# Performance work log

Hardware: AMD Instinct MI355X
Metric: run time of the kernel (lower is better)

## Reference

```python
import jax, jax.numpy as jnp
import numpy as np

THRESH = 0.3
VRESET = 0.0
TAU_M = 3.0
MAX_D = 5
LENS = 0.5  # surrogate-gradient window half-width

B, WIN, N_IN = 512, 100, 700
H1, H2, H3 = 512, 256, 128

@jax.custom_vjp
def spike_fn(mem):
    # Heaviside spike with rectangular surrogate gradient (standard ActFun in SNN repos)
    return (mem > THRESH).astype(mem.dtype)

def _spike_fwd(mem):
    return spike_fn(mem), mem

def _spike_bwd(mem, g):
    return (g * (jnp.abs(mem - THRESH) < LENS).astype(g.dtype),)

spike_fn.defvjp(_spike_fwd, _spike_bwd)


def mem_update(i_spike, o_spike, mem, W, alpha):
    # mem = mem*alpha*(1-o_spike) + W @ i_spike - o_spike*vreset
    mem = mem * alpha * (1.0 - o_spike) + i_spike @ W.T - o_spike * VRESET
    s = spike_fn(mem)
    mem = mem * (mem < THRESH).astype(mem.dtype)  # hard reset above threshold
    return mem, s


def setup_inputs() -> dict:
    key = jax.random.key(0)
    ks = jax.random.split(key, 7)
    x = (jax.random.uniform(ks[0], (B, WIN, N_IN), jnp.float32) > 0.9).astype(jnp.float32)

    def lin(k, fan_out, fan_in):
        bound = 1.0 / np.sqrt(fan_in)
        return jax.random.uniform(k, (fan_out, fan_in), jnp.float32, -bound, bound)

    return {
        "x": x,
        "W_ih1": lin(ks[1], H1, N_IN),
        "W_h1h2": lin(ks[2], H2, H1),
        "W_h2h3": lin(ks[3], H3, H2),
        "W_h3h2": lin(ks[4], H2, H3),
        "W_h2h1": lin(ks[5], H1, H2),
        "W_h1o": lin(ks[6], N_IN, H1),
    }


def reference(x, W_ih1, W_h1h2, W_h2h3, W_h3h2, W_h2h1, W_h1o):
    b, t, n = x.shape
    alpha = jnp.exp(jnp.asarray(-1.0 / TAU_M, x.dtype))
    ext = jnp.concatenate([jnp.zeros((b, MAX_D, n), x.dtype), x], axis=1)  # [B, T+max_d, N]
    xs = jnp.swapaxes(ext, 0, 1)  # [T+max_d, B, N]

    z = lambda d: jnp.zeros((b, d), x.dtype)
    carry0 = (z(H1), z(H1), z(H2), z(H2), z(H3), z(H3),
              z(H2), z(H2), z(H1), z(H1), z(n), z(n))

    def step(carry, xt):
        m1, s1, m2, s2, m3, s3, m2d, s2d, m1d, s1d, mo, so = carry
        m1, s1 = mem_update(xt, s1, m1, W_ih1, alpha)
        m2, s2 = mem_update(s1, s2, m2, W_h1h2, alpha)
        m3, s3 = mem_update(s2, s3, m3, W_h2h3, alpha)
        m2d, s2d = mem_update(s3, s2d, m2d, W_h3h2, alpha)
        m1d, s1d = mem_update(s2d, s1d, m1d, W_h2h1, alpha)
        mo, so = mem_update(s1d, so, mo, W_h1o, alpha)
        return (m1, s1, m2, s2, m3, s3, m2d, s2d, m1d, s1d, mo, so), so

    _, all_o = jax.lax.scan(step, carry0, xs)  # [T+max_d, B, N]
    return jnp.swapaxes(all_o[MAX_D:], 0, 1)   # [B, T, N]
```

## Files before the change

kernel.cpp:

```cpp
#include <hip/hip_runtime.h>
#include <cmath>

namespace {

constexpr int kWin = 100;
constexpr int kNin = 700;

constexpr size_t OFF1 = 0;
constexpr size_t OFF2 = 358400;
constexpr size_t OFF3 = 489472;
constexpr size_t OFF4 = 522240;
constexpr size_t OFF5 = 555008;
constexpr size_t OFF6 = 686080;
constexpr size_t OFF_END = 1044480;
constexpr size_t XM_OFF_U64 = OFF_END / 2;

__global__ void transpose_k(const float* __restrict__ src, float* __restrict__ dst,
                            int H, int K) {
  int idx = blockIdx.x * blockDim.x + threadIdx.x;
  if (idx < H * K) {
    int h = idx / K;
    int k = idx - h * K;
    dst[(size_t)k * H + h] = src[idx];
  }
}

__global__ __launch_bounds__(256) void xmask_k(const float* __restrict__ x,
                                               unsigned long long* __restrict__ xm) {
  const int bid = blockIdx.x;
  const int tid = threadIdx.x;
  const int lane = tid & 63;
  const int wv = tid >> 6;
  const float* xr = x + (size_t)bid * kNin;
  unsigned long long* dst = xm + (size_t)bid * 12;
#pragma unroll
  for (int s = 0; s < 3; ++s) {
    const int h = s * 256 + tid;
    const bool p = (h < kNin) ? (xr[h] != 0.0f) : false;
    const unsigned long long b = __ballot(p);
    if (lane == 0) dst[s * 4 + wv] = b;
  }
}

template <int K, int H, bool BUILD, typename FCh>
__device__ __forceinline__ void lif(const float* __restrict__ WT, FCh&& chunk,
                                    double* mem, unsigned long long* mOut,
                                    double (*part)[3][256],
                                    float* outRow,
                                    int kp, int ht, int lane, int wv4,
                                    double alpha) {
  constexpr int NS = (H + 255) / 256;
  constexpr int NC = (K + 31) / 32;
  double acc[NS];
#pragma unroll
  for (int s = 0; s < NS; ++s) acc[s] = 0.0;

  unsigned mNext = chunk(kp);
  for (int c = kp; c < NC; c += 4) {
    unsigned m = __builtin_amdgcn_readfirstlane(mNext);
    if (c + 4 < NC) mNext = chunk(c + 4);
    const float* __restrict__ cbase = WT + (size_t)c * 32 * H;
    const int cnt = __builtin_popcount(m);
    int i = 0;
    for (; i + 4 <= cnt; i += 4) {
      const int b0 = __builtin_ctz(m); m &= m - 1;
      const int b1 = __builtin_ctz(m); m &= m - 1;
      const int b2 = __builtin_ctz(m); m &= m - 1;
      const int b3 = __builtin_ctz(m); m &= m - 1;
      const float* p0 = cbase + b0 * H;
      const float* p1 = cbase + b1 * H;
      const float* p2 = cbase + b2 * H;
      const float* p3 = cbase + b3 * H;
#pragma unroll
      for (int s = 0; s < NS; ++s) {
        const int h = s * 256 + ht;
        if ((s + 1) * 256 <= H || h < H) {
          const float f0 = p0[h];
          const float f1 = p1[h];
          const float f2 = p2[h];
          const float f3 = p3[h];
          const double t01 = (double)f0 + (double)f1;
          const double t23 = (double)f2 + (double)f3;
          acc[s] += t01 + t23;
        }
      }
    }
    for (; i < cnt; ++i) {
      const int b0 = __builtin_ctz(m); m &= m - 1;
      const float* p0 = cbase + b0 * H;
#pragma unroll
      for (int s = 0; s < NS; ++s) {
        const int h = s * 256 + ht;
        if ((s + 1) * 256 <= H || h < H) acc[s] += (double)p0[h];
      }
    }
  }

#pragma unroll
  for (int s = 0; s < NS; ++s) part[kp][s][ht] = acc[s];
  __syncthreads();

  bool pred[NS];
#pragma unroll
  for (int s = 0; s < NS; ++s) {
    const int h = s * 256 + ht;
    if ((s + 1) * 256 <= H || h < H) {
      const double p01 = part[0][s][ht] + part[1][s][ht];
      const double tot = (p01 + part[2][s][ht]) + part[3][s][ht];
      const double mm = mem[s] * alpha + tot;
      pred[s] = (mm > 0.3);
      mem[s] = (mm < 0.3) ? mm : 0.0;
      if (!BUILD) {
        if (kp == s) outRow[h] = pred[s] ? 1.0f : 0.0f;
      }
    } else {
      pred[s] = false;
    }
  }
  if (BUILD) {
#pragma unroll
    for (int s = 0; s < NS; ++s) {
      const unsigned long long b = __ballot(pred[s]);
      if (kp == 0 && lane == 0) mOut[s * 4 + wv4] = b;
    }
    __syncthreads();
  }
}

__global__ __launch_bounds__(1024, 8) void snn_main(
    const float* __restrict__ wsf, const unsigned long long* __restrict__ xmask,
    float* __restrict__ out) {
  const int tid = threadIdx.x;
  const int kp = tid >> 8;
  const int ht = tid & 255;
  const int lane = tid & 63;
  const int wv4 = (tid >> 6) & 3;
  const int row = blockIdx.x;

  const float* WT1 = wsf + OFF1;
  const float* WT2 = wsf + OFF2;
  const float* WT3 = wsf + OFF3;
  const float* WT4 = wsf + OFF4;
  const float* WT5 = wsf + OFF5;
  const float* WT6 = wsf + OFF6;

  __shared__ unsigned long long mk[2][12];
  __shared__ double parts[2][4][3][256];

  double m1[2] = {0.0, 0.0};
  double m2[1] = {0.0};
  double m3[1] = {0.0};
  double m4[1] = {0.0};
  double m5[2] = {0.0, 0.0};
  double m6[3] = {0.0, 0.0, 0.0};

  const double alpha = exp(-1.0 / 3.0);

  const unsigned long long* xmRow = xmask + (size_t)row * kWin * 12;
  float* outRowBase = out + (size_t)row * kWin * kNin;

  for (int t = 0; t < kWin; ++t) {
    const unsigned* xm32 = (const unsigned*)(xmRow + (size_t)t * 12);
    const unsigned* mk0 = (const unsigned*)&mk[0][0];
    const unsigned* mk1 = (const unsigned*)&mk[1][0];

    lif<700, 512, true>(WT1, [&](int c) { return xm32[c]; }, m1, mk[0],
                        parts[0], nullptr, kp, ht, lane, wv4, alpha);
    lif<512, 256, true>(WT2, [&](int c) { return mk0[c]; }, m2, mk[1],
                        parts[1], nullptr, kp, ht, lane, wv4, alpha);
    lif<256, 128, true>(WT3, [&](int c) { return mk1[c]; }, m3, mk[0],
                        parts[0], nullptr, kp, ht, lane, wv4, alpha);
    lif<128, 256, true>(WT4, [&](int c) { return mk0[c]; }, m4, mk[1],
                        parts[1], nullptr, kp, ht, lane, wv4, alpha);
    lif<256, 512, true>(WT5, [&](int c) { return mk1[c]; }, m5, mk[0],
                        parts[0], nullptr, kp, ht, lane, wv4, alpha);
    float* outRow = outRowBase + (size_t)t * kNin;
    lif<512, 700, false>(WT6, [&](int c) { return mk0[c]; }, m6, nullptr,
                         parts[1], outRow, kp, ht, lane, wv4, alpha);
  }
}

}

extern "C" void kernel_launch(void* const* d_in, const int* in_sizes, int n_in,
                              void* d_out, int out_size, void* d_ws, size_t ws_size,
                              hipStream_t stream) {
  const float* x = (const float*)d_in[0];
  float* ws = (float*)d_ws;
  unsigned long long* xm = (unsigned long long*)d_ws + XM_OFF_U64;
  float* out = (float*)d_out;

  struct TK { int H, K; size_t off; int idx; };
  const TK tk[6] = {
      {512, 700, OFF1, 1},
      {256, 512, OFF2, 2},
      {128, 256, OFF3, 3},
      {256, 128, OFF4, 4},
      {512, 256, OFF5, 5},
      {700, 512, OFF6, 6},
  };
  for (int i = 0; i < 6; ++i) {
    const int n = tk[i].H * tk[i].K;
    transpose_k<<<(n + 255) / 256, 256, 0, stream>>>(
        (const float*)d_in[tk[i].idx], ws + tk[i].off, tk[i].H, tk[i].K);
  }

  xmask_k<<<512 * kWin, 256, 0, stream>>>(x, xm);

  snn_main<<<512, 1024, 0, stream>>>(ws, xm, out);
}
```

Measured before the change: 1.141 ms.

## Balance sparse spike work across K-partitions by splitting active rows evenly

Each of the four K-partition thread groups now takes an equal share of the active spike indices, replacing the earlier round-robin assignment of 32-bit chunks, which could leave groups with very different amounts of work. Spike counts are computed with popcounts when the masks are built, and the last word of the input mask is reused to hold the total count. In exchange, every group now scans all mask chunks from the start, and the bit-skipping loops add scalar work per layer per timestep.

```diff
diff --git a/kernel.cpp b/kernel.cpp
--- a/kernel.cpp
+++ b/kernel.cpp
@@ -33,18 +33,28 @@
   const int wv = tid >> 6;
   const float* xr = x + (size_t)bid * kNin;
   unsigned long long* dst = xm + (size_t)bid * 12;
+  __shared__ int sc[4];
+  int tc = 0;
 #pragma unroll
   for (int s = 0; s < 3; ++s) {
     const int h = s * 256 + tid;
     const bool p = (h < kNin) ? (xr[h] != 0.0f) : false;
     const unsigned long long b = __ballot(p);
-    if (lane == 0) dst[s * 4 + wv] = b;
-  }
+    const int idx = s * 4 + wv;
+    tc += (int)__popcll(b);
+    if (lane == 0 && idx < 11) dst[idx] = b;
+  }
+  if (lane == 0) sc[wv] = tc;
+  __syncthreads();
+  if (tid == 0)
+    dst[11] = (unsigned long long)((sc[0] + sc[1]) + (sc[2] + sc[3]));
 }
 
 template <int K, int H, bool BUILD, typename FCh>
 __device__ __forceinline__ void lif(const float* __restrict__ WT, FCh&& chunk,
+                                    int tot,
                                     double* mem, unsigned long long* mOut,
+                                    int* mcOut,
                                     double (*part)[3][256],
                                     float* outRow,
                                     int kp, int ht, int lane, int wv4,
@@ -55,14 +65,28 @@
 #pragma unroll
   for (int s = 0; s < NS; ++s) acc[s] = 0.0;
 
-  unsigned mNext = chunk(kp);
-  for (int c = kp; c < NC; c += 4) {
+  const int Q = (tot + 3) >> 2;
+  const int rlo = kp * Q;
+  const int rhiA = rlo + Q;
+  const int rhi = (rhiA < tot) ? rhiA : tot;
+
+  unsigned mNext = chunk(0);
+  int cum = 0;
+  for (int c = 0; c < NC && cum < rhi; ++c) {
     unsigned m = __builtin_amdgcn_readfirstlane(mNext);
-    if (c + 4 < NC) mNext = chunk(c + 4);
+    if (c + 1 < NC) mNext = chunk(c + 1);
+    const int pc = __builtin_popcount(m);
+    const int lo = (cum > rlo) ? cum : rlo;
+    const int hiA = cum + pc;
+    const int hi = (hiA < rhi) ? hiA : rhi;
+    cum = hiA;
+    if (lo >= hi) continue;
+    const int nskip = lo - (hiA - pc);
+    for (int i = 0; i < nskip; ++i) m &= m - 1;
+    const int n = hi - lo;
     const float* __restrict__ cbase = WT + (size_t)c * 32 * H;
-    const int cnt = __builtin_popcount(m);
     int i = 0;
-    for (; i + 4 <= cnt; i += 4) {
+    for (; i + 4 <= n; i += 4) {
       const int b0 = __builtin_ctz(m); m &= m - 1;
       const int b1 = __builtin_ctz(m); m &= m - 1;
       const int b2 = __builtin_ctz(m); m &= m - 1;
@@ -85,7 +109,7 @@
         }
       }
     }
-    for (; i < cnt; ++i) {
+    for (; i < n; ++i) {
       const int b0 = __builtin_ctz(m); m &= m - 1;
       const float* p0 = cbase + b0 * H;
 #pragma unroll
@@ -106,8 +130,8 @@
     const int h = s * 256 + ht;
     if ((s + 1) * 256 <= H || h < H) {
       const double p01 = part[0][s][ht] + part[1][s][ht];
-      const double tot = (p01 + part[2][s][ht]) + part[3][s][ht];
-      const double mm = mem[s] * alpha + tot;
+      const double tot2 = (p01 + part[2][s][ht]) + part[3][s][ht];
+      const double mm = mem[s] * alpha + tot2;
       pred[s] = (mm > 0.3);
       mem[s] = (mm < 0.3) ? mm : 0.0;
       if (!BUILD) {
@@ -118,11 +142,14 @@
     }
   }
   if (BUILD) {
+    int cw = 0;
 #pragma unroll
     for (int s = 0; s < NS; ++s) {
       const unsigned long long b = __ballot(pred[s]);
+      cw += (int)__popcll(b);
       if (kp == 0 && lane == 0) mOut[s * 4 + wv4] = b;
     }
+    if (kp == 0 && lane == 0) mcOut[wv4] = cw;
     __syncthreads();
   }
 }
@@ -144,7 +171,8 @@
   const float* WT5 = wsf + OFF5;
   const float* WT6 = wsf + OFF6;
 
-  __shared__ unsigned long long mk[2][12];
+  __shared__ alignas(16) unsigned long long mk[2][12];
+  __shared__ alignas(16) int mc[2][4];
   __shared__ double parts[2][4][3][256];
 
   double m1[2] = {0.0, 0.0};
@@ -164,19 +192,40 @@
     const unsigned* mk0 = (const unsigned*)&mk[0][0];
     const unsigned* mk1 = (const unsigned*)&mk[1][0];
 
-    lif<700, 512, true>(WT1, [&](int c) { return xm32[c]; }, m1, mk[0],
-                        parts[0], nullptr, kp, ht, lane, wv4, alpha);
-    lif<512, 256, true>(WT2, [&](int c) { return mk0[c]; }, m2, mk[1],
-                        parts[1], nullptr, kp, ht, lane, wv4, alpha);
-    lif<256, 128, true>(WT3, [&](int c) { return mk1[c]; }, m3, mk[0],
-                        parts[0], nullptr, kp, ht, lane, wv4, alpha);
-    lif<128, 256, true>(WT4, [&](int c) { return mk0[c]; }, m4, mk[1],
-                        parts[1], nullptr, kp, ht, lane, wv4, alpha);
-    lif<256, 512, true>(WT5, [&](int c) { return mk1[c]; }, m5, mk[0],
-                        parts[0], nullptr, kp, ht, lane, wv4, alpha);
-    float* outRow = outRowBase + (size_t)t * kNin;
-    lif<512, 700, false>(WT6, [&](int c) { return mk0[c]; }, m6, nullptr,
-                         parts[1], outRow, kp, ht, lane, wv4, alpha);
+    const int totX = (int)xm32[22];
+    lif<700, 512, true>(WT1, [&](int c) { return xm32[c]; }, totX, m1, mk[0],
+                        mc[0], parts[0], nullptr, kp, ht, lane, wv4, alpha);
+    {
+      const int4 v = *(const int4*)&mc[0][0];
+      lif<512, 256, true>(WT2, [&](int c) { return mk0[c]; },
+                          (v.x + v.y) + (v.z + v.w), m2, mk[1], mc[1],
+                          parts[1], nullptr, kp, ht, lane, wv4, alpha);
+    }
+    {
+      const int4 v = *(const int4*)&mc[1][0];
+      lif<256, 128, true>(WT3, [&](int c) { return mk1[c]; },
+                          (v.x + v.y) + (v.z + v.w), m3, mk[0], mc[0],
+                          parts[0], nullptr, kp, ht, lane, wv4, alpha);
+    }
+    {
+      const int4 v = *(const int4*)&mc[0][0];
+      lif<128, 256, true>(WT4, [&](int c) { return mk0[c]; },
+                          (v.x + v.y) + (v.z + v.w), m4, mk[1], mc[1],
+                          parts[1], nullptr, kp, ht, lane, wv4, alpha);
+    }
+    {
+      const int4 v = *(const int4*)&mc[1][0];
+      lif<256, 512, true>(WT5, [&](int c) { return mk1[c]; },
+                          (v.x + v.y) + (v.z + v.w), m5, mk[0], mc[0],
+                          parts[0], nullptr, kp, ht, lane, wv4, alpha);
+    }
+    {
+      const int4 v = *(const int4*)&mc[0][0];
+      float* outRow = outRowBase + (size_t)t * kNin;
+      lif<512, 700, false>(WT6, [&](int c) { return mk0[c]; },
+                           (v.x + v.y) + (v.z + v.w), m6, nullptr, nullptr,
+                           parts[1], outRow, kp, ht, lane, wv4, alpha);
+    }
   }
 }
 
```

After: 2.147 ms. 88.1% more time.

## Replace spike bitmasks with compacted active-index lists balanced across k-partitions

Applied to the files above, without the earlier changes.

Each layer now emits a compacted list of active neuron indices (premultiplied row offsets) built with ballot, popcount and a shared atomic counter, instead of a bitmask. The accumulation loop splits that list evenly across the four k-partition wave groups, where before each group took fixed 32-bit chunks, so sparse spikes are spread more evenly across groups. The next timestep's input list is built inside layer 5 to hide its latency. The costs are shared-memory atomics and extra counter resets, and the accumulation order becomes nondeterministic, though the sums stay in double precision.

```diff
diff --git a/kernel.cpp b/kernel.cpp
--- a/kernel.cpp
+++ b/kernel.cpp
@@ -42,56 +42,70 @@
   }
 }
 
-template <int K, int H, bool BUILD, typename FCh>
-__device__ __forceinline__ void lif(const float* __restrict__ WT, FCh&& chunk,
-                                    double* mem, unsigned long long* mOut,
+template <int H, int HNEXT, bool BUILD, bool XB>
+__device__ __forceinline__ void lif(const float* __restrict__ WT,
+                                    const int* __restrict__ listIn,
+                                    const int* __restrict__ cntIn,
+                                    int* __restrict__ listOut,
+                                    int* __restrict__ cntOut,
                                     double (*part)[3][256],
-                                    float* outRow,
-                                    int kp, int ht, int lane, int wv4,
-                                    double alpha) {
+                                    double* mem, double alpha,
+                                    float* __restrict__ outRow,
+                                    unsigned long long xw, bool doX,
+                                    int* __restrict__ xList,
+                                    int* __restrict__ xCnt,
+                                    int kp, int ht, int lane, int wv4, int w) {
   constexpr int NS = (H + 255) / 256;
-  constexpr int NC = (K + 31) / 32;
   double acc[NS];
 #pragma unroll
   for (int s = 0; s < NS; ++s) acc[s] = 0.0;
 
-  unsigned mNext = chunk(kp);
-  for (int c = kp; c < NC; c += 4) {
-    unsigned m = __builtin_amdgcn_readfirstlane(mNext);
-    if (c + 4 < NC) mNext = chunk(c + 4);
-    const float* __restrict__ cbase = WT + (size_t)c * 32 * H;
-    const int cnt = __builtin_popcount(m);
-    int i = 0;
-    for (; i + 4 <= cnt; i += 4) {
-      const int b0 = __builtin_ctz(m); m &= m - 1;
-      const int b1 = __builtin_ctz(m); m &= m - 1;
-      const int b2 = __builtin_ctz(m); m &= m - 1;
-      const int b3 = __builtin_ctz(m); m &= m - 1;
-      const float* p0 = cbase + b0 * H;
-      const float* p1 = cbase + b1 * H;
-      const float* p2 = cbase + b2 * H;
-      const float* p3 = cbase + b3 * H;
+  const int cnt = __builtin_amdgcn_readfirstlane(*cntIn);
+  const int qlen = ((cnt + 15) >> 4) << 2;
+  const int start = kp * qlen;
+  const int endA = start + qlen;
+  const int end = (endA < cnt) ? endA : cnt;
+  const float* __restrict__ wbase = WT + ht;
+  if (start < end) {
+    const int n4 = (end - start) & ~3;
+    const int e4 = start + n4;
+    int j = start;
+    if (n4 > 0) {
+      int4 eC = *(const int4*)(listIn + j);
+      for (; j < e4; j += 4) {
+        const int jn = (j + 4 < e4) ? (j + 4) : j;
+        int4 eN = *(const int4*)(listIn + jn);
+        const int e0 = __builtin_amdgcn_readfirstlane(eC.x);
+        const int e1 = __builtin_amdgcn_readfirstlane(eC.y);
+        const int e2 = __builtin_amdgcn_readfirstlane(eC.z);
+        const int e3 = __builtin_amdgcn_readfirstlane(eC.w);
+        const float* p0 = wbase + e0;
+        const float* p1 = wbase + e1;
+        const float* p2 = wbase + e2;
+        const float* p3 = wbase + e3;
+#pragma unroll
+        for (int s = 0; s < NS; ++s) {
+          const int h = s * 256 + ht;
+          if ((s + 1) * 256 <= H || h < H) {
+            const float f0 = p0[s * 256];
+            const float f1 = p1[s * 256];
+            const float f2 = p2[s * 256];
+            const float f3 = p3[s * 256];
+            const double t01 = (double)f0 + (double)f1;
+            const double t23 = (double)f2 + (double)f3;
+            acc[s] += t01 + t23;
+          }
+        }
+        eC = eN;
+      }
+    }
+    for (; j < end; ++j) {
+      const int e0 = __builtin_amdgcn_readfirstlane(listIn[j]);
+      const float* p0 = wbase + e0;
 #pragma unroll
       for (int s = 0; s < NS; ++s) {
         const int h = s * 256 + ht;
-        if ((s + 1) * 256 <= H || h < H) {
-          const float f0 = p0[h];
-          const float f1 = p1[h];
-          const float f2 = p2[h];
-          const float f3 = p3[h];
-          const double t01 = (double)f0 + (double)f1;
-          const double t23 = (double)f2 + (double)f3;
-          acc[s] += t01 + t23;
-        }
-      }
-    }
-    for (; i < cnt; ++i) {
-      const int b0 = __builtin_ctz(m); m &= m - 1;
-      const float* p0 = cbase + b0 * H;
-#pragma unroll
-      for (int s = 0; s < NS; ++s) {
-        const int h = s * 256 + ht;
-        if ((s + 1) * 256 <= H || h < H) acc[s] += (double)p0[h];
+        if ((s + 1) * 256 <= H || h < H) acc[s] += (double)p0[s * 256];
       }
     }
   }
@@ -117,14 +131,36 @@
       pred[s] = false;
     }
   }
+  const unsigned long long lt = (1ull << lane) - 1ull;
   if (BUILD) {
 #pragma unroll
     for (int s = 0; s < NS; ++s) {
       const unsigned long long b = __ballot(pred[s]);
-      if (kp == 0 && lane == 0) mOut[s * 4 + wv4] = b;
-    }
-    __syncthreads();
-  }
+      if (kp == 0) {
+        const int n = (int)__popcll(b);
+        int base = 0;
+        if (lane == 0 && n > 0) base = atomicAdd(cntOut, n);
+        base = __shfl(base, 0);
+        if (pred[s]) {
+          const int rank = (int)__popcll(b & lt);
+          listOut[base + rank] = (s * 256 + ht) * HNEXT;
+        }
+      }
+    }
+  }
+  if (XB) {
+    if (doX && w < 11) {
+      const int n = (int)__popcll(xw);
+      int base = 0;
+      if (lane == 0 && n > 0) base = atomicAdd(xCnt, n);
+      base = __shfl(base, 0);
+      if ((xw >> lane) & 1ull) {
+        const int rank = (int)__popcll(xw & lt);
+        xList[base + rank] = (w * 64 + lane) * 512;
+      }
+    }
+  }
+  if (BUILD) __syncthreads();
 }
 
 __global__ __launch_bounds__(1024, 8) void snn_main(
@@ -135,6 +171,7 @@
   const int ht = tid & 255;
   const int lane = tid & 63;
   const int wv4 = (tid >> 6) & 3;
+  const int w = tid >> 6;
   const int row = blockIdx.x;
 
   const float* WT1 = wsf + OFF1;
@@ -144,8 +181,11 @@
   const float* WT5 = wsf + OFF5;
   const float* WT6 = wsf + OFF6;
 
-  __shared__ unsigned long long mk[2][12];
   __shared__ double parts[2][4][3][256];
+  __shared__ alignas(16) int hL[2][512];
+  __shared__ alignas(16) int inL[2][704];
+  __shared__ int cH[2];
+  __shared__ int inCnt[2];
 
   double m1[2] = {0.0, 0.0};
   double m2[1] = {0.0};
@@ -155,28 +195,57 @@
   double m6[3] = {0.0, 0.0, 0.0};
 
   const double alpha = exp(-1.0 / 3.0);
+  const unsigned long long lt = (1ull << lane) - 1ull;
 
   const unsigned long long* xmRow = xmask + (size_t)row * kWin * 12;
   float* outRowBase = out + (size_t)row * kWin * kNin;
 
+  unsigned long long b0 = 0;
+  if (w < 11) b0 = xmRow[w];
+  if (tid == 0) { cH[0] = 0; cH[1] = 0; inCnt[0] = 0; inCnt[1] = 0; }
+  __syncthreads();
+  if (w < 11) {
+    const int n = (int)__popcll(b0);
+    int base = 0;
+    if (lane == 0 && n > 0) base = atomicAdd(&inCnt[0], n);
+    base = __shfl(base, 0);
+    if ((b0 >> lane) & 1ull) {
+      const int rank = (int)__popcll(b0 & lt);
+      inL[0][base + rank] = (w * 64 + lane) * 512;
+    }
+  }
+  __syncthreads();
+
   for (int t = 0; t < kWin; ++t) {
-    const unsigned* xm32 = (const unsigned*)(xmRow + (size_t)t * 12);
-    const unsigned* mk0 = (const unsigned*)&mk[0][0];
-    const unsigned* mk1 = (const unsigned*)&mk[1][0];
-
-    lif<700, 512, true>(WT1, [&](int c) { return xm32[c]; }, m1, mk[0],
-                        parts[0], nullptr, kp, ht, lane, wv4, alpha);
-    lif<512, 256, true>(WT2, [&](int c) { return mk0[c]; }, m2, mk[1],
-                        parts[1], nullptr, kp, ht, lane, wv4, alpha);
-    lif<256, 128, true>(WT3, [&](int c) { return mk1[c]; }, m3, mk[0],
-                        parts[0], nullptr, kp, ht, lane, wv4, alpha);
-    lif<128, 256, true>(WT4, [&](int c) { return mk0[c]; }, m4, mk[1],
-                        parts[1], nullptr, kp, ht, lane, wv4, alpha);
-    lif<256, 512, true>(WT5, [&](int c) { return mk1[c]; }, m5, mk[0],
-                        parts[0], nullptr, kp, ht, lane, wv4, alpha);
+    const bool doX = (t + 1 < kWin);
+    unsigned long long xw = 0;
+    if (w < 11) xw = xmRow[(size_t)(doX ? (t + 1) : t) * 12 + w];
+
+    lif<512, 256, true, false>(WT1, inL[t & 1], &inCnt[t & 1], hL[0], &cH[0],
+                               parts[0], m1, alpha, nullptr, 0, false, nullptr,
+                               nullptr, kp, ht, lane, wv4, w);
+    lif<256, 128, true, false>(WT2, hL[0], &cH[0], hL[1], &cH[1],
+                               parts[1], m2, alpha, nullptr, 0, false, nullptr,
+                               nullptr, kp, ht, lane, wv4, w);
+    if (tid == 0) cH[0] = 0;
+    lif<128, 256, true, false>(WT3, hL[1], &cH[1], hL[0], &cH[0],
+                               parts[0], m3, alpha, nullptr, 0, false, nullptr,
+                               nullptr, kp, ht, lane, wv4, w);
+    if (tid == 0) cH[1] = 0;
+    lif<256, 512, true, false>(WT4, hL[0], &cH[0], hL[1], &cH[1],
+                               parts[1], m4, alpha, nullptr, 0, false, nullptr,
+                               nullptr, kp, ht, lane, wv4, w);
+    if (tid == 0) { cH[0] = 0; inCnt[(t + 1) & 1] = 0; }
+    lif<512, 700, true, true>(WT5, hL[1], &cH[1], hL[0], &cH[0],
+                              parts[0], m5, alpha, nullptr, xw, doX,
+                              inL[(t + 1) & 1], &inCnt[(t + 1) & 1],
+                              kp, ht, lane, wv4, w);
+    if (tid == 0) cH[1] = 0;
     float* outRow = outRowBase + (size_t)t * kNin;
-    lif<512, 700, false>(WT6, [&](int c) { return mk0[c]; }, m6, nullptr,
-                         parts[1], outRow, kp, ht, lane, wv4, alpha);
+    lif<700, 1, false, false>(WT6, hL[0], &cH[0], nullptr, nullptr,
+                              parts[1], m6, alpha, outRow, 0, false, nullptr,
+                              nullptr, kp, ht, lane, wv4, w);
+    if (tid == 0) cH[0] = 0;
   }
 }
 
```

After: 1.268 ms. 1.11x slower.
